# Performance work log

Hardware: AMD Instinct MI355X
Metric: run time of the kernel (lower is better)

Reference implementation:

```python
import jax, jax.numpy as jnp
import numpy as np

B, N, M, C = 4, 4096, 4096, 256
IMG_W, IMG_H = 1280.0, 384.0


def setup_inputs() -> dict:
    key = jax.random.key(0)
    ks = jax.random.split(key, 12)
    nodes_L = jax.random.normal(ks[0], (B, N, C), dtype=jnp.float32)
    nodes_R = jax.random.normal(ks[1], (B, M, C), dtype=jnp.float32)
    # pixel coordinates: (u, v) with u in [0, IMG_W), v in [0, IMG_H)
    scale = jnp.array([IMG_W, IMG_H], dtype=jnp.float32)
    kpts_L = jax.random.uniform(ks[2], (B, N, 2), dtype=jnp.float32) * scale
    kpts_R = jax.random.uniform(ks[3], (B, M, 2), dtype=jnp.float32) * scale
    s = 1.0 / np.sqrt(C)
    Wq = jax.random.normal(ks[4], (C, C), dtype=jnp.float32) * s
    bq = jnp.zeros((C,), dtype=jnp.float32)
    Wk = jax.random.normal(ks[5], (C, C), dtype=jnp.float32) * s
    bk = jnp.zeros((C,), dtype=jnp.float32)
    Wv = jax.random.normal(ks[6], (C, C), dtype=jnp.float32) * s
    bv = jnp.zeros((C,), dtype=jnp.float32)
    Wm = jax.random.normal(ks[7], (C, C), dtype=jnp.float32) * s
    bm = jnp.zeros((C,), dtype=jnp.float32)
    return {"nodes_L": nodes_L, "nodes_R": nodes_R, "kpts_L": kpts_L, "kpts_R": kpts_R,
            "Wq": Wq, "bq": bq, "Wk": Wk, "bk": bk, "Wv": Wv, "bv": bv, "Wm": Wm, "bm": bm}


def reference(nodes_L, nodes_R, kpts_L, kpts_R, Wq, bq, Wk, bk, Wv, bv, Wm, bm):
    dim = nodes_L.shape[-1]
    # torch Linear: x @ W.T + b
    Q = nodes_L @ Wq.T + bq                      # [B,N,C]
    K = nodes_R @ Wk.T + bk                      # [B,M,C]
    V = nodes_R @ Wv.T + bv                      # [B,M,C]
    # epipolar geometry terms, [B,N,M]
    dist_v = jnp.abs(kpts_L[:, :, 1:2] - kpts_R[:, :, 1][:, None, :])
    dist_u = kpts_L[:, :, 0:1] - kpts_R[:, :, 0][:, None, :]
    mask = (dist_v < 3.0) & (dist_u > 0) & (dist_u < 192)
    attn = jnp.einsum('bnc,bmc->bnm', Q, K) / jnp.sqrt(jnp.float32(dim))
    attn = jnp.where(mask, attn, jnp.float32(-1e9))
    attn_weights = jax.nn.softmax(attn, axis=-1)  # [B,N,M]
    matched = jnp.einsum('bnm,bmc->bnc', attn_weights, V)
    init_disparity = jnp.sum(attn_weights * dist_u, axis=-1, keepdims=True)  # [B,N,1]
    confidence = jnp.any(mask, axis=-1, keepdims=True).astype(jnp.float32)   # [B,N,1]
    return matched @ Wm.T + bm, init_disparity, confidence
```

## Files before the change

### kernel.cpp

```cpp
#include <hip/hip_runtime.h>
#include <hip/hip_bf16.h>

#define BB 4
#define NN 4096
#define MM 4096
#define CC 256
#define CAP 128
#define NBIN 384
#define NCH 16
#define CHK 256

typedef __attribute__((ext_vector_type(8))) short bf16x8;
typedef __attribute__((ext_vector_type(4))) float f32x4;

static __device__ __forceinline__ float bf2f(unsigned short u) {
    return __uint_as_float(((unsigned)u) << 16);
}
static __device__ __forceinline__ unsigned short f2bf(float f) {
    unsigned u = __float_as_uint(f);
    u += 0x7fffu + ((u >> 16) & 1u);
    return (unsigned short)(u >> 16);
}
static __device__ __forceinline__ bf16x8 asbf(uint4 u) {
    union { uint4 a; bf16x8 b; } c; c.a = u; return c.b;
}
static __device__ __forceinline__ void gload16(const unsigned short* g, unsigned short* l) {
    __builtin_amdgcn_global_load_lds(
        (const __attribute__((address_space(1))) unsigned int*)g,
        (__attribute__((address_space(3))) unsigned int*)l, 16, 0, 0);
}

__global__ __launch_bounds__(256) void prep_kernel(
    const float* __restrict__ Wq, const float* __restrict__ Wk,
    const float* __restrict__ Wv, const float* __restrict__ Wm,
    const float* __restrict__ L, const float* __restrict__ R,
    const float* __restrict__ kptsR, const float* __restrict__ kptsL,
    unsigned short* __restrict__ Wpk, unsigned short* __restrict__ Lpk,
    unsigned short* __restrict__ Rpk,
    int* __restrict__ hist, unsigned short* __restrict__ prank,
    int* __restrict__ histL, unsigned short* __restrict__ prankL,
    float* __restrict__ Vsum, float* __restrict__ Usum)
{
    __shared__ __align__(16) unsigned char SMEM[32768];
    const int tid = threadIdx.x, y = blockIdx.y, x = blockIdx.x;

    if (y < 4) {
        const float* S = (y == 0) ? Wq : (y == 1) ? Wk : (y == 2) ? Wv : Wm;
        int o = x * 256 + tid;
        int j = o & 7, lane = (o >> 3) & 63, kt = o >> 9;
        int kk = kt >> 4, t = kt & 15;
        int r = t * 16 + (lane & 15), c = kk * 32 + (lane >> 4) * 8 + j;
        Wpk[(size_t)y * 65536 + o] = f2bf(S[r * 256 + c]);
        return;
    }
    if (y < 6) {
        const float* S = (y == 5) ? R : L;
        unsigned short* D = (y == 5) ? Rpk : Lpk;
        unsigned short* T = (unsigned short*)SMEM;
        const int wid = tid >> 6, lane = tid & 63;
        const size_t R0 = (size_t)x * 64;
#pragma unroll
        for (int it = 0; it < 16; ++it) {
            int row = it * 4 + wid;
            float4 f = *(const float4*)(S + (R0 + row) * 256 + lane * 4);
            ushort4 h = make_ushort4(f2bf(f.x), f2bf(f.y), f2bf(f.z), f2bf(f.w));
            int col = lane * 4;
            *(ushort4*)&T[row * 256 + (col ^ ((row & 7) << 3))] = h;
        }
        __syncthreads();
        unsigned short* Dp = D + (size_t)x * 16384;
#pragma unroll
        for (int p = 0; p < 8; ++p) {
            int u = p * 2048 + tid * 8;
            int rt = u >> 12, rem = u & 4095;
            int kk = rem >> 9, ln = (rem >> 3) & 63;
            int row = rt * 16 + (ln & 15);
            int col = kk * 32 + (ln >> 4) * 8;
            *(uint4*)(Dp + u) = *(const uint4*)&T[row * 256 + (col ^ ((row & 7) << 3))];
        }
        return;
    }
    if (y == 6 || y == 8) {
        if (x >= NCH * BB) return;
        const float* KP = (y == 8) ? kptsL : kptsR;
        int* H = (y == 8) ? histL : hist;
        unsigned short* PR = (y == 8) ? prankL : prank;
        int chunk = x & 15, b = x >> 4;
        int* h = (int*)SMEM;
        short* sbin = (short*)(SMEM + NBIN * 4);
        for (int i = tid; i < NBIN; i += CHK) h[i] = 0;
        int m = chunk * CHK + tid;
        float2 p = ((const float2*)KP)[(size_t)b * MM + m];
        int bin = (int)p.y;
        sbin[tid] = (short)bin;
        __syncthreads();
        atomicAdd(&h[bin], 1);
        int r = 0;
        for (int t = 0; t < tid; ++t) r += (sbin[t] == bin);
        PR[(b << 12) + m] = (unsigned short)r;
        __syncthreads();
        for (int i = tid; i < NBIN; i += CHK)
            H[((size_t)b * NCH + chunk) * NBIN + i] = h[i];
        return;
    }
    if (x < BB) {
        int b = x;
        float s = 0.f;
        for (int m = tid; m < MM; m += 256) s += kptsR[((size_t)b * MM + m) * 2 + 0];
#pragma unroll
        for (int off = 32; off; off >>= 1) s += __shfl_xor(s, off);
        float* sr = (float*)SMEM;
        int wave = tid >> 6, lane = tid & 63;
        if (lane == 0) sr[wave] = s;
        __syncthreads();
        if (tid == 0) Usum[b] = sr[0] + sr[1] + sr[2] + sr[3];
    } else if (x == BB) {
        for (int i = tid; i < BB * CC; i += 256) Vsum[i] = 0.f;
    }
}

template <bool OUT_BF16>
__global__ __launch_bounds__(256, 4) void proj_mfma_kernel(
    const unsigned short* __restrict__ A0, const unsigned short* __restrict__ A1,
    const unsigned short* __restrict__ A2, const unsigned short* __restrict__ Wpk,
    const float* __restrict__ b0, const float* __restrict__ b1, const float* __restrict__ b2,
    void* __restrict__ O0, void* __restrict__ O1, void* __restrict__ O2,
    float* __restrict__ Vsum,
    const int* __restrict__ hist, const int* __restrict__ histL,
    int* __restrict__ binStart,
    const float* __restrict__ kptsR, const float* __restrict__ kptsL,
    const unsigned short* __restrict__ prank, const unsigned short* __restrict__ prankL,
    unsigned short* __restrict__ sortedM, float2* __restrict__ sortedUV,
    unsigned short* __restrict__ sortedNL)
{
    __shared__ __align__(16) unsigned char SMEM[32768];
    const int tid = threadIdx.x, wid = tid >> 6, lane = tid & 63;
    const int y = blockIdx.y;

    if (y == 3) {
        if (blockIdx.x >= 2 * NCH * BB) return;
        const int isL = blockIdx.x >= NCH * BB;
        const int xx = blockIdx.x & (NCH * BB - 1);
        const int b = xx >> 4, chunk = xx & 15;
        const int* H = isL ? histL : hist;
        int* h2 = (int*)SMEM;
        int* sc = (int*)(SMEM + 24576);
        for (int i = tid; i < NCH * NBIN; i += 256)
            h2[i] = H[(size_t)b * NCH * NBIN + i];
        __syncthreads();
        for (int v = tid; v < NBIN; v += 256) {
            int tot = 0;
#pragma unroll
            for (int c = 0; c < NCH; ++c) tot += h2[c * NBIN + v];
            sc[v] = tot;
        }
        __syncthreads();
        for (int off = 1; off < NBIN; off <<= 1) {
            int v1 = tid + 256;
            int t0 = (tid >= off) ? sc[tid - off] : 0;
            int t1 = (v1 < NBIN && v1 >= off) ? sc[v1 - off] : 0;
            __syncthreads();
            sc[tid] += t0;
            if (v1 < NBIN) sc[v1] += t1;
            __syncthreads();
        }
        if (!isL && chunk == 0) {
            for (int v = tid; v < NBIN; v += 256)
                binStart[b * (NBIN + 1) + v] = v ? sc[v - 1] : 0;
            if (tid == 0) binStart[b * (NBIN + 1) + NBIN] = sc[NBIN - 1];
        }
        int m = chunk * CHK + tid;
        float2 p = ((const float2*)(isL ? kptsL : kptsR))[(size_t)b * MM + m];
        int bin = (int)p.y;
        int ex = bin ? sc[bin - 1] : 0;
        for (int c = 0; c < chunk; ++c) ex += h2[c * NBIN + bin];
        int pos = ex + (isL ? prankL : prank)[(b << 12) + m];
        if (isL) {
            sortedNL[(b << 12) + pos] = (unsigned short)m;
        } else {
            sortedM[(b << 12) + pos] = (unsigned short)m;
            sortedUV[(b << 12) + pos] = p;
        }
        return;
    }

    const int lrow = lane & 15, lk = lane >> 4;
    const unsigned short* A = (y == 0) ? A0 : (y == 1) ? A1 : A2;
    const float* bias = (y == 0) ? b0 : (y == 1) ? b1 : b2;
    void* Out = (y == 0) ? O0 : (y == 1) ? O1 : O2;
    const unsigned short* W = Wpk + (size_t)y * 65536;

    const int bid = blockIdx.x;
    const int g = (bid >> 3) & 3;
    const int rblk = (bid & 7) + ((bid >> 5) << 3);
    const size_t rbase = (size_t)rblk * 128;
    const int rt0 = rblk * 8 + wid * 2;

    unsigned short* Wl = (unsigned short*)SMEM;
#pragma unroll
    for (int i = 0; i < 8; ++i) {
        int kk = wid * 2 + (i >> 2), q = i & 3;
        gload16(W + (size_t)kk * 8192 + g * 2048 + q * 512 + lane * 8,
                Wl + kk * 2048 + q * 512 + lane * 8);
    }

    const unsigned short* Ap = A + (size_t)rt0 * 4096 + lane * 8;
    uint4 a[2][2];
    a[0][0] = *(const uint4*)(Ap);
    a[0][1] = *(const uint4*)(Ap + 4096);

    f32x4 acc[4][2];
#pragma unroll
    for (int t = 0; t < 4; ++t) {
        acc[t][0] = (f32x4){0.f, 0.f, 0.f, 0.f};
        acc[t][1] = (f32x4){0.f, 0.f, 0.f, 0.f};
    }

    asm volatile("s_waitcnt vmcnt(0)" ::: "memory");
    __syncthreads();

#pragma unroll
    for (int kk = 0; kk < 8; ++kk) {
        const int cur = kk & 1, nxt = cur ^ 1;
        if (kk < 7) {
            a[nxt][0] = *(const uint4*)(Ap + (kk + 1) * 512);
            a[nxt][1] = *(const uint4*)(Ap + 4096 + (kk + 1) * 512);
        }
        bf16x8 af0 = asbf(a[cur][0]);
        bf16x8 af1 = asbf(a[cur][1]);
#pragma unroll
        for (int t = 0; t < 4; ++t) {
            bf16x8 wf = *(const bf16x8*)(Wl + kk * 2048 + t * 512 + lane * 8);
            acc[t][0] = __builtin_amdgcn_mfma_f32_16x16x32_bf16(af0, wf, acc[t][0], 0, 0, 0);
            acc[t][1] = __builtin_amdgcn_mfma_f32_16x16x32_bf16(af1, wf, acc[t][1], 0, 0, 0);
        }
    }

    if (Vsum != nullptr && y == 2) {
#pragma unroll
        for (int t = 0; t < 4; ++t) {
            int col = g * 64 + t * 16 + lrow;
            float vs = acc[t][0][0] + acc[t][0][1] + acc[t][0][2] + acc[t][0][3]
                     + acc[t][1][0] + acc[t][1][1] + acc[t][1][2] + acc[t][1][3];
            vs += __shfl_xor(vs, 16);
            vs += __shfl_xor(vs, 32);
            if (lk == 0)
                atomicAdd(&Vsum[(rblk >> 5) * CC + col], vs + 32.f * bias[col]);
        }
    }

    __syncthreads();
    if constexpr (OUT_BF16) {
        unsigned short* Bo = (unsigned short*)SMEM;
#pragma unroll
        for (int t = 0; t < 4; ++t) {
            float bb = bias[g * 64 + t * 16 + lrow];
#pragma unroll
            for (int s = 0; s < 2; ++s)
#pragma unroll
                for (int rr = 0; rr < 4; ++rr) {
                    int row = wid * 32 + s * 16 + lk * 4 + rr;
                    Bo[row * 64 + t * 16 + lrow] = f2bf(acc[t][s][rr] + bb);
                }
        }
        __syncthreads();
        unsigned short* O = (unsigned short*)Out;
#pragma unroll
        for (int it = 0; it < 4; ++it) {
            int idx = it * 2048 + tid * 8;
            int row = idx >> 6, col = idx & 63;
            *(uint4*)(O + (rbase + row) * CC + g * 64 + col) = *(const uint4*)&Bo[idx];
        }
    } else {
        float* Bo = (float*)SMEM;
#pragma unroll
        for (int t = 0; t < 4; ++t) {
            float bb = bias[g * 64 + t * 16 + lrow];
#pragma unroll
            for (int s = 0; s < 2; ++s)
#pragma unroll
                for (int rr = 0; rr < 4; ++rr) {
                    int row = wid * 32 + s * 16 + lk * 4 + rr;
                    Bo[row * 64 + t * 16 + lrow] = acc[t][s][rr] + bb;
                }
        }
        __syncthreads();
        float* O = (float*)Out;
#pragma unroll
        for (int it = 0; it < 8; ++it) {
            int idx = it * 1024 + tid * 4;
            int row = idx >> 6, col = idx & 63;
            *(float4*)(O + (rbase + row) * CC + g * 64 + col) = *(const float4*)&Bo[idx];
        }
    }
}

static __device__ __forceinline__ size_t mt_po(int bn, int lane) {
    return ((size_t)(bn >> 4)) * 4096 + (size_t)(lane >> 3) * 512
         + (size_t)(((lane >> 1) & 3) * 16 + (bn & 15)) * 8 + (lane & 1) * 4;
}

__global__ __launch_bounds__(256) void attn_kernel(
    const unsigned short* __restrict__ Q, const unsigned short* __restrict__ K,
    const unsigned short* __restrict__ V,
    const float* __restrict__ kptsL, const unsigned short* __restrict__ sortedNL,
    const int* __restrict__ binStart, const unsigned short* __restrict__ sortedM,
    const float2* __restrict__ sortedUV,
    const float* __restrict__ Vsum, const float* __restrict__ Usum,
    unsigned short* __restrict__ Mpk, float* __restrict__ out1, float* __restrict__ out2)
{
    __shared__ unsigned short s_m[4][CAP];
    __shared__ float s_du[4][CAP];
    __shared__ float s_p[4][CAP];

    const int wid = threadIdx.x >> 6, lane = threadIdx.x & 63;
    const int bid = (blockIdx.x & 7) * 512 + (blockIdx.x >> 3);
    const int si = bid * 4 + wid;
    const int b = si >> 12;
    const int bn = (b << 12) + sortedNL[si];

    const int gi = lane >> 4, c = lane & 15;
    float qf[16];
    {
        const unsigned short* Qr = Q + (size_t)bn * CC + c * 16;
#pragma unroll
        for (int j = 0; j < 4; ++j) {
            ushort4 t = *(const ushort4*)(Qr + j * 4);
            qf[j * 4 + 0] = bf2f(t.x); qf[j * 4 + 1] = bf2f(t.y);
            qf[j * 4 + 2] = bf2f(t.z); qf[j * 4 + 3] = bf2f(t.w);
        }
    }

    float2 kl = *(const float2*)(kptsL + (size_t)bn * 2);
    float uL = kl.x, vL = kl.y;

    int ifl = (int)vL;
    int v0 = max(0, ifl - 3), v1 = min(NBIN - 1, ifl + 3);
    int s = binStart[b * (NBIN + 1) + v0];
    int e = binStart[b * (NBIN + 1) + v1 + 1];

    int cnt = 0;
    for (int i0 = s; i0 < e; i0 += 64) {
        int i = i0 + lane;
        bool valid = false;
        float du = 0.f;
        int m = 0;
        if (i < e) {
            float2 uv = sortedUV[(b << 12) + i];
            m = sortedM[(b << 12) + i];
            du = uL - uv.x;
            float dv = fabsf(vL - uv.y);
            valid = (dv < 3.0f) && (du > 0.0f) && (du < 192.0f);
        }
        unsigned long long bal = __ballot(valid);
        int pos = cnt + __popcll(bal & ((1ull << lane) - 1ull));
        if (valid && pos < CAP) { s_m[wid][pos] = (unsigned short)m; s_du[wid][pos] = du; }
        cnt += __popcll(bal);
    }
    if (cnt > CAP) cnt = CAP;

    if (cnt == 0) {
        float4 vs = *(const float4*)(Vsum + b * CC + lane * 4);
        ushort4 o = make_ushort4(f2bf(vs.x * (1.f / MM)), f2bf(vs.y * (1.f / MM)),
                                 f2bf(vs.z * (1.f / MM)), f2bf(vs.w * (1.f / MM)));
        *(ushort4*)(Mpk + mt_po(bn, lane)) = o;
        if (lane == 0) { out1[bn] = uL - Usum[b] * (1.f / MM); out2[bn] = 0.f; }
        return;
    }

    const unsigned short* Kb = K + (((size_t)b) << 12) * CC;
    for (int i0 = 0; i0 < cnt; i0 += 4) {
        int i = i0 + gi;
        int m = s_m[wid][(i < cnt) ? i : 0];
        const unsigned short* Kr = Kb + (size_t)m * CC + c * 16;
        float d = 0.f;
#pragma unroll
        for (int j = 0; j < 4; ++j) {
            ushort4 t = *(const ushort4*)(Kr + j * 4);
            d += qf[j * 4 + 0] * bf2f(t.x) + qf[j * 4 + 1] * bf2f(t.y)
               + qf[j * 4 + 2] * bf2f(t.z) + qf[j * 4 + 3] * bf2f(t.w);
        }
        d += __shfl_xor(d, 8); d += __shfl_xor(d, 4);
        d += __shfl_xor(d, 2); d += __shfl_xor(d, 1);
        if (c == 0 && i < cnt) s_p[wid][i] = d;
    }

    const float NEG = -3.0e38f;
    float mx, ps, ds, inv;
    if (cnt <= 64) {
        float x0 = (lane < cnt) ? s_p[wid][lane] * 0.0625f : NEG;
        mx = x0;
#pragma unroll
        for (int off = 32; off; off >>= 1) mx = fmaxf(mx, __shfl_xor(mx, off));
        float p0 = (lane < cnt) ? __expf(x0 - mx) : 0.f;
        float d0 = (lane < cnt) ? s_du[wid][lane] : 0.f;
        ps = p0; ds = p0 * d0;
#pragma unroll
        for (int off = 32; off; off >>= 1) { ps += __shfl_xor(ps, off); ds += __shfl_xor(ds, off); }
        inv = 1.f / ps;
        if (lane < cnt) s_p[wid][lane] = p0 * inv;
    } else {
        float x0 = (lane < cnt) ? s_p[wid][lane] * 0.0625f : NEG;
        float x1 = (lane + 64 < cnt) ? s_p[wid][lane + 64] * 0.0625f : NEG;
        mx = fmaxf(x0, x1);
#pragma unroll
        for (int off = 32; off; off >>= 1) mx = fmaxf(mx, __shfl_xor(mx, off));
        float p0 = (lane < cnt) ? __expf(x0 - mx) : 0.f;
        float p1 = (lane + 64 < cnt) ? __expf(x1 - mx) : 0.f;
        float d0 = (lane < cnt) ? s_du[wid][lane] : 0.f;
        float d1 = (lane + 64 < cnt) ? s_du[wid][lane + 64] : 0.f;
        ps = p0 + p1; ds = p0 * d0 + p1 * d1;
#pragma unroll
        for (int off = 32; off; off >>= 1) { ps += __shfl_xor(ps, off); ds += __shfl_xor(ds, off); }
        inv = 1.f / ps;
        if (lane < cnt) s_p[wid][lane] = p0 * inv;
        if (lane + 64 < cnt) s_p[wid][lane + 64] = p1 * inv;
    }

    const unsigned short* Vb = V + (((size_t)b) << 12) * CC;
    float a0 = 0.f, a1 = 0.f, a2 = 0.f, a3 = 0.f;
    float e0 = 0.f, e1 = 0.f, e2 = 0.f, e3 = 0.f;
    int i = 0;
    for (; i + 1 < cnt; i += 2) {
        float w0 = s_p[wid][i], w1 = s_p[wid][i + 1];
        ushort4 va = *(const ushort4*)(Vb + (size_t)s_m[wid][i] * CC + lane * 4);
        ushort4 vb = *(const ushort4*)(Vb + (size_t)s_m[wid][i + 1] * CC + lane * 4);
        a0 += w0 * bf2f(va.x); a1 += w0 * bf2f(va.y);
        a2 += w0 * bf2f(va.z); a3 += w0 * bf2f(va.w);
        e0 += w1 * bf2f(vb.x); e1 += w1 * bf2f(vb.y);
        e2 += w1 * bf2f(vb.z); e3 += w1 * bf2f(vb.w);
    }
    if (i < cnt) {
        float w0 = s_p[wid][i];
        ushort4 va = *(const ushort4*)(Vb + (size_t)s_m[wid][i] * CC + lane * 4);
        a0 += w0 * bf2f(va.x); a1 += w0 * bf2f(va.y);
        a2 += w0 * bf2f(va.z); a3 += w0 * bf2f(va.w);
    }
    ushort4 o = make_ushort4(f2bf(a0 + e0), f2bf(a1 + e1), f2bf(a2 + e2), f2bf(a3 + e3));
    *(ushort4*)(Mpk + mt_po(bn, lane)) = o;
    if (lane == 0) { out1[bn] = ds * inv; out2[bn] = 1.f; }
}

extern "C" void kernel_launch(void* const* d_in, const int* in_sizes, int n_in,
                              void* d_out, int out_size, void* d_ws, size_t ws_size,
                              hipStream_t stream) {
    const float* nodes_L = (const float*)d_in[0];
    const float* nodes_R = (const float*)d_in[1];
    const float* kpts_L  = (const float*)d_in[2];
    const float* kpts_R  = (const float*)d_in[3];
    const float* Wq = (const float*)d_in[4];
    const float* bq = (const float*)d_in[5];
    const float* Wk = (const float*)d_in[6];
    const float* bk = (const float*)d_in[7];
    const float* Wv = (const float*)d_in[8];
    const float* bv = (const float*)d_in[9];
    const float* Wm = (const float*)d_in[10];
    const float* bm = (const float*)d_in[11];

    char* ws = (char*)d_ws;
    unsigned short* Wpk = (unsigned short*)ws; ws += (size_t)4 * 65536 * 2;
    unsigned short* Lpk = (unsigned short*)ws; ws += (size_t)BB * NN * CC * 2;
    unsigned short* Rpk = (unsigned short*)ws; ws += (size_t)BB * MM * CC * 2;
    unsigned short* Qp  = (unsigned short*)ws; ws += (size_t)BB * NN * CC * 2;
    unsigned short* Kp  = (unsigned short*)ws; ws += (size_t)BB * MM * CC * 2;
    unsigned short* Vp  = (unsigned short*)ws; ws += (size_t)BB * MM * CC * 2;
    unsigned short* Mpk = (unsigned short*)ws; ws += (size_t)BB * NN * CC * 2;
    float* Vsum = (float*)ws;        ws += (size_t)BB * CC * 4;
    float* Usum = (float*)ws;        ws += (size_t)BB * 4;
    float2* sortedUV = (float2*)ws;  ws += (size_t)BB * MM * 8;
    int* binStart = (int*)ws;        ws += (size_t)BB * (NBIN + 1) * 4;
    unsigned short* sortedM = (unsigned short*)ws; ws += (size_t)BB * MM * 2;
    int* hist = (int*)ws;            ws += (size_t)BB * NCH * NBIN * 4;
    unsigned short* prank = (unsigned short*)ws;   ws += (size_t)BB * MM * 2;
    int* histL = (int*)ws;           ws += (size_t)BB * NCH * NBIN * 4;
    unsigned short* prankL = (unsigned short*)ws;  ws += (size_t)BB * NN * 2;
    unsigned short* sortedNL = (unsigned short*)ws;

    float* out0 = (float*)d_out;
    float* out1 = out0 + (size_t)BB * NN * CC;
    float* out2 = out1 + (size_t)BB * NN;

    prep_kernel<<<dim3(256, 9), dim3(256), 0, stream>>>(
        Wq, Wk, Wv, Wm, nodes_L, nodes_R, kpts_R, kpts_L,
        Wpk, Lpk, Rpk, hist, prank, histL, prankL, Vsum, Usum);

    proj_mfma_kernel<true><<<dim3(512, 4), dim3(256), 0, stream>>>(
        Lpk, Rpk, Rpk, Wpk, bq, bk, bv, Qp, Kp, Vp, Vsum,
        hist, histL, binStart, kpts_R, kpts_L, prank, prankL,
        sortedM, sortedUV, sortedNL);

    attn_kernel<<<dim3(BB * NN / 4), dim3(256), 0, stream>>>(
        Qp, Kp, Vp, kpts_L, sortedNL, binStart, sortedM, sortedUV,
        Vsum, Usum, Mpk, out1, out2);

    proj_mfma_kernel<false><<<dim3(512, 1), dim3(256), 0, stream>>>(
        Mpk, nullptr, nullptr, Wpk + 3 * 65536, bm, nullptr, nullptr,
        out0, nullptr, nullptr, nullptr,
        nullptr, nullptr, nullptr, nullptr, nullptr, nullptr, nullptr,
        nullptr, nullptr, nullptr);
}
```

Measured before the change: 60.53 us.

## Fuse fp32-to-bf16 input conversion into QKV projection kernel

```diff
diff --git a/kernel.cpp b/kernel.cpp
--- a/kernel.cpp
+++ b/kernel.cpp
@@ -33,15 +33,13 @@
 __global__ __launch_bounds__(256) void prep_kernel(
     const float* __restrict__ Wq, const float* __restrict__ Wk,
     const float* __restrict__ Wv, const float* __restrict__ Wm,
-    const float* __restrict__ L, const float* __restrict__ R,
     const float* __restrict__ kptsR, const float* __restrict__ kptsL,
-    unsigned short* __restrict__ Wpk, unsigned short* __restrict__ Lpk,
-    unsigned short* __restrict__ Rpk,
+    unsigned short* __restrict__ Wpk,
     int* __restrict__ hist, unsigned short* __restrict__ prank,
     int* __restrict__ histL, unsigned short* __restrict__ prankL,
     float* __restrict__ Vsum, float* __restrict__ Usum)
 {
-    __shared__ __align__(16) unsigned char SMEM[32768];
+    __shared__ __align__(16) unsigned char SMEM[2048];
     const int tid = threadIdx.x, y = blockIdx.y, x = blockIdx.x;
 
     if (y < 4) {
@@ -53,41 +51,14 @@
         Wpk[(size_t)y * 65536 + o] = f2bf(S[r * 256 + c]);
         return;
     }
-    if (y < 6) {
-        const float* S = (y == 5) ? R : L;
-        unsigned short* D = (y == 5) ? Rpk : Lpk;
-        unsigned short* T = (unsigned short*)SMEM;
-        const int wid = tid >> 6, lane = tid & 63;
-        const size_t R0 = (size_t)x * 64;
-#pragma unroll
-        for (int it = 0; it < 16; ++it) {
-            int row = it * 4 + wid;
-            float4 f = *(const float4*)(S + (R0 + row) * 256 + lane * 4);
-            ushort4 h = make_ushort4(f2bf(f.x), f2bf(f.y), f2bf(f.z), f2bf(f.w));
-            int col = lane * 4;
-            *(ushort4*)&T[row * 256 + (col ^ ((row & 7) << 3))] = h;
-        }
-        __syncthreads();
-        unsigned short* Dp = D + (size_t)x * 16384;
-#pragma unroll
-        for (int p = 0; p < 8; ++p) {
-            int u = p * 2048 + tid * 8;
-            int rt = u >> 12, rem = u & 4095;
-            int kk = rem >> 9, ln = (rem >> 3) & 63;
-            int row = rt * 16 + (ln & 15);
-            int col = kk * 32 + (ln >> 4) * 8;
-            *(uint4*)(Dp + u) = *(const uint4*)&T[row * 256 + (col ^ ((row & 7) << 3))];
-        }
-        return;
-    }
-    if (y == 6 || y == 8) {
+    if (y == 4 || y == 5) {
         if (x >= NCH * BB) return;
-        const float* KP = (y == 8) ? kptsL : kptsR;
-        int* H = (y == 8) ? histL : hist;
-        unsigned short* PR = (y == 8) ? prankL : prank;
+        __shared__ int h[NBIN];
+        __shared__ short sbin[CHK];
+        const float* KP = (y == 5) ? kptsL : kptsR;
+        int* H = (y == 5) ? histL : hist;
+        unsigned short* PR = (y == 5) ? prankL : prank;
         int chunk = x & 15, b = x >> 4;
-        int* h = (int*)SMEM;
-        short* sbin = (short*)(SMEM + NBIN * 4);
         for (int i = tid; i < NBIN; i += CHK) h[i] = 0;
         int m = chunk * CHK + tid;
         float2 p = ((const float2*)KP)[(size_t)b * MM + m];
@@ -119,13 +90,12 @@
     }
 }
 
-template <bool OUT_BF16>
-__global__ __launch_bounds__(256, 4) void proj_mfma_kernel(
-    const unsigned short* __restrict__ A0, const unsigned short* __restrict__ A1,
-    const unsigned short* __restrict__ A2, const unsigned short* __restrict__ Wpk,
+__global__ __launch_bounds__(256, 2) void qkv_mfma_kernel(
+    const float* __restrict__ A0, const float* __restrict__ A1,
+    const float* __restrict__ A2, const unsigned short* __restrict__ Wpk,
     const float* __restrict__ b0, const float* __restrict__ b1, const float* __restrict__ b2,
-    void* __restrict__ O0, void* __restrict__ O1, void* __restrict__ O2,
-    float* __restrict__ Vsum,
+    unsigned short* __restrict__ O0, unsigned short* __restrict__ O1,
+    unsigned short* __restrict__ O2, float* __restrict__ Vsum,
     const int* __restrict__ hist, const int* __restrict__ histL,
     int* __restrict__ binStart,
     const float* __restrict__ kptsR, const float* __restrict__ kptsL,
@@ -133,7 +103,7 @@
     unsigned short* __restrict__ sortedM, float2* __restrict__ sortedUV,
     unsigned short* __restrict__ sortedNL)
 {
-    __shared__ __align__(16) unsigned char SMEM[32768];
+    __shared__ __align__(16) unsigned char SMEM[65536];
     const int tid = threadIdx.x, wid = tid >> 6, lane = tid & 63;
     const int y = blockIdx.y;
 
@@ -185,10 +155,93 @@
     }
 
     const int lrow = lane & 15, lk = lane >> 4;
-    const unsigned short* A = (y == 0) ? A0 : (y == 1) ? A1 : A2;
+    const float* A = (y == 0) ? A0 : (y == 1) ? A1 : A2;
     const float* bias = (y == 0) ? b0 : (y == 1) ? b1 : b2;
-    void* Out = (y == 0) ? O0 : (y == 1) ? O1 : O2;
+    unsigned short* Out = (y == 0) ? O0 : (y == 1) ? O1 : O2;
     const unsigned short* W = Wpk + (size_t)y * 65536;
+
+    const int bid = blockIdx.x;
+    const int g = (bid >> 3) & 3;
+    const int rblk = (bid & 7) + ((bid >> 5) << 3);
+    const size_t rbase = (size_t)rblk * 64;
+
+    unsigned short* Al = (unsigned short*)SMEM;
+    unsigned short* Wl = (unsigned short*)(SMEM + 32768);
+
+#pragma unroll
+    for (int i = 0; i < 8; ++i) {
+        int kk = wid * 2 + (i >> 2), q = i & 3;
+        gload16(W + (size_t)kk * 8192 + g * 2048 + q * 512 + lane * 8,
+                Wl + kk * 2048 + q * 512 + lane * 8);
+    }
+
+    const float* Af = A + rbase * CC;
+#pragma unroll
+    for (int it = 0; it < 16; ++it) {
+        int row = it * 4 + wid;
+        float4 f = *(const float4*)(Af + row * 256 + lane * 4);
+        ushort4 h = make_ushort4(f2bf(f.x), f2bf(f.y), f2bf(f.z), f2bf(f.w));
+        *(ushort4*)&Al[row * 256 + ((lane * 4) ^ ((row & 7) << 3))] = h;
+    }
+
+    f32x4 acc[4];
+#pragma unroll
+    for (int t = 0; t < 4; ++t) acc[t] = (f32x4){0.f, 0.f, 0.f, 0.f};
+
+    asm volatile("s_waitcnt vmcnt(0)" ::: "memory");
+    __syncthreads();
+
+    const int arow = wid * 16 + lrow;
+    const int xr = (arow & 7) << 3;
+#pragma unroll
+    for (int kk = 0; kk < 8; ++kk) {
+        bf16x8 a = *(const bf16x8*)&Al[arow * 256 + ((kk * 32 + lk * 8) ^ xr)];
+#pragma unroll
+        for (int t = 0; t < 4; ++t) {
+            bf16x8 wf = *(const bf16x8*)&Wl[kk * 2048 + t * 512 + lane * 8];
+            acc[t] = __builtin_amdgcn_mfma_f32_16x16x32_bf16(a, wf, acc[t], 0, 0, 0);
+        }
+    }
+
+    if (y == 2) {
+#pragma unroll
+        for (int t = 0; t < 4; ++t) {
+            int col = g * 64 + t * 16 + lrow;
+            float vs = acc[t][0] + acc[t][1] + acc[t][2] + acc[t][3];
+            vs += __shfl_xor(vs, 16);
+            vs += __shfl_xor(vs, 32);
+            if (lk == 0)
+                atomicAdd(&Vsum[(rblk >> 6) * CC + col], vs + 16.f * bias[col]);
+        }
+    }
+
+    __syncthreads();
+    unsigned short* Bo = (unsigned short*)SMEM;
+#pragma unroll
+    for (int t = 0; t < 4; ++t) {
+        float bb = bias[g * 64 + t * 16 + lrow];
+#pragma unroll
+        for (int rr = 0; rr < 4; ++rr) {
+            int row = wid * 16 + lk * 4 + rr;
+            Bo[row * 64 + t * 16 + lrow] = f2bf(acc[t][rr] + bb);
+        }
+    }
+    __syncthreads();
+#pragma unroll
+    for (int it = 0; it < 2; ++it) {
+        int idx = it * 2048 + tid * 8;
+        int row = idx >> 6, col = idx & 63;
+        *(uint4*)(Out + (rbase + row) * CC + g * 64 + col) = *(const uint4*)&Bo[idx];
+    }
+}
+
+__global__ __launch_bounds__(256, 4) void proj_mfma_kernel(
+    const unsigned short* __restrict__ A, const unsigned short* __restrict__ Wpk,
+    const float* __restrict__ bias, float* __restrict__ Out)
+{
+    __shared__ __align__(16) unsigned char SMEM[32768];
+    const int tid = threadIdx.x, wid = tid >> 6, lane = tid & 63;
+    const int lrow = lane & 15, lk = lane >> 4;
 
     const int bid = blockIdx.x;
     const int g = (bid >> 3) & 3;
@@ -200,7 +253,7 @@
 #pragma unroll
     for (int i = 0; i < 8; ++i) {
         int kk = wid * 2 + (i >> 2), q = i & 3;
-        gload16(W + (size_t)kk * 8192 + g * 2048 + q * 512 + lane * 8,
+        gload16(Wpk + (size_t)kk * 8192 + g * 2048 + q * 512 + lane * 8,
                 Wl + kk * 2048 + q * 512 + lane * 8);
     }
 
@@ -236,62 +289,33 @@
         }
     }
 
-    if (Vsum != nullptr && y == 2) {
-#pragma unroll
-        for (int t = 0; t < 4; ++t) {
-            int col = g * 64 + t * 16 + lrow;
-            float vs = acc[t][0][0] + acc[t][0][1] + acc[t][0][2] + acc[t][0][3]
-                     + acc[t][1][0] + acc[t][1][1] + acc[t][1][2] + acc[t][1][3];
-            vs += __shfl_xor(vs, 16);
-            vs += __shfl_xor(vs, 32);
-            if (lk == 0)
-                atomicAdd(&Vsum[(rblk >> 5) * CC + col], vs + 32.f * bias[col]);
-        }
-    }
-
     __syncthreads();
-    if constexpr (OUT_BF16) {
-        unsigned short* Bo = (unsigned short*)SMEM;
+    float* Bo = (float*)SMEM;
+#pragma unroll
+    for (int half = 0; half < 2; ++half) {
 #pragma unroll
         for (int t = 0; t < 4; ++t) {
             float bb = bias[g * 64 + t * 16 + lrow];
 #pragma unroll
-            for (int s = 0; s < 2; ++s)
-#pragma unroll
-                for (int rr = 0; rr < 4; ++rr) {
-                    int row = wid * 32 + s * 16 + lk * 4 + rr;
-                    Bo[row * 64 + t * 16 + lrow] = f2bf(acc[t][s][rr] + bb);
-                }
-        }
-        __syncthreads();
-        unsigned short* O = (unsigned short*)Out;
-#pragma unroll
-        for (int it = 0; it < 4; ++it) {
-            int idx = it * 2048 + tid * 8;
-            int row = idx >> 6, col = idx & 63;
-            *(uint4*)(O + (rbase + row) * CC + g * 64 + col) = *(const uint4*)&Bo[idx];
-        }
-    } else {
-        float* Bo = (float*)SMEM;
-#pragma unroll
-        for (int t = 0; t < 4; ++t) {
-            float bb = bias[g * 64 + t * 16 + lrow];
-#pragma unroll
-            for (int s = 0; s < 2; ++s)
-#pragma unroll
-                for (int rr = 0; rr < 4; ++rr) {
-                    int row = wid * 32 + s * 16 + lk * 4 + rr;
-                    Bo[row * 64 + t * 16 + lrow] = acc[t][s][rr] + bb;
-                }
-        }
-        __syncthreads();
-        float* O = (float*)Out;
-#pragma unroll
-        for (int it = 0; it < 8; ++it) {
-            int idx = it * 1024 + tid * 4;
-            int row = idx >> 6, col = idx & 63;
-            *(float4*)(O + (rbase + row) * CC + g * 64 + col) = *(const float4*)&Bo[idx];
-        }
+            for (int rr = 0; rr < 4; ++rr) {
+                int row = wid * 32 + half * 16 + lk * 4 + rr;
+                if ((row >> 6) == half)
+                    Bo[(row & 63) * 64 + t * 16 + lrow] = acc[t][half][rr] + bb;
+            }
+        }
+        __syncthreads();
+        __syncthreads();
+    }
+#pragma unroll
+    for (int t = 0; t < 4; ++t) {
+        float bb = bias[g * 64 + t * 16 + lrow];
+#pragma unroll
+        for (int s = 0; s < 2; ++s)
+#pragma unroll
+            for (int rr = 0; rr < 4; ++rr) {
+                int row = wid * 32 + s * 16 + lk * 4 + rr;
+                Out[(rbase + row) * CC + g * 64 + t * 16 + lrow] = acc[t][s][rr] + bb;
+            }
     }
 }
 
@@ -459,8 +483,6 @@
 
     char* ws = (char*)d_ws;
     unsigned short* Wpk = (unsigned short*)ws; ws += (size_t)4 * 65536 * 2;
-    unsigned short* Lpk = (unsigned short*)ws; ws += (size_t)BB * NN * CC * 2;
-    unsigned short* Rpk = (unsigned short*)ws; ws += (size_t)BB * MM * CC * 2;
     unsigned short* Qp  = (unsigned short*)ws; ws += (size_t)BB * NN * CC * 2;
     unsigned short* Kp  = (unsigned short*)ws; ws += (size_t)BB * MM * CC * 2;
     unsigned short* Vp  = (unsigned short*)ws; ws += (size_t)BB * MM * CC * 2;
@@ -480,12 +502,12 @@
     float* out1 = out0 + (size_t)BB * NN * CC;
     float* out2 = out1 + (size_t)BB * NN;
 
-    prep_kernel<<<dim3(256, 9), dim3(256), 0, stream>>>(
-        Wq, Wk, Wv, Wm, nodes_L, nodes_R, kpts_R, kpts_L,
-        Wpk, Lpk, Rpk, hist, prank, histL, prankL, Vsum, Usum);
-
-    proj_mfma_kernel<true><<<dim3(512, 4), dim3(256), 0, stream>>>(
-        Lpk, Rpk, Rpk, Wpk, bq, bk, bv, Qp, Kp, Vp, Vsum,
+    prep_kernel<<<dim3(256, 7), dim3(256), 0, stream>>>(
+        Wq, Wk, Wv, Wm, kpts_R, kpts_L,
+        Wpk, hist, prank, histL, prankL, Vsum, Usum);
+
+    qkv_mfma_kernel<<<dim3(1024, 4), dim3(256), 0, stream>>>(
+        nodes_L, nodes_R, nodes_R, Wpk, bq, bk, bv, Qp, Kp, Vp, Vsum,
         hist, histL, binStart, kpts_R, kpts_L, prank, prankL,
         sortedM, sortedUV, sortedNL);
 
@@ -493,9 +515,6 @@
         Qp, Kp, Vp, kpts_L, sortedNL, binStart, sortedM, sortedUV,
         Vsum, Usum, Mpk, out1, out2);
 
-    proj_mfma_kernel<false><<<dim3(512, 1), dim3(256), 0, stream>>>(
-        Mpk, nullptr, nullptr, Wpk + 3 * 65536, bm, nullptr, nullptr,
-        out0, nullptr, nullptr, nullptr,
-        nullptr, nullptr, nullptr, nullptr, nullptr, nullptr, nullptr,
-        nullptr, nullptr, nullptr);
-}
+    proj_mfma_kernel<<<dim3(512, 1), dim3(256), 0, stream>>>(
+        Mpk, Wpk + 3 * 65536, bm, out0);
+}
```

Result: slower. 78.89 us (+30.3%).
